# Performance work log

Hardware: AMD Instinct MI355X
Metric: run time of the kernel (lower is better)

Reference implementation:

```python
import jax, jax.numpy as jnp
import numpy as np
import math

BS, C, NH, NL, NP = 2, 128, 1, 2, 8
SHAPES = np.array([[128, 256], [64, 128]], dtype=np.int64)  # [num_level, (H, W)]
NQ = int(SHAPES[0, 0] * SHAPES[0, 1])  # 32768 queries at level-0 resolution
NV = int((SHAPES[:, 0] * SHAPES[:, 1]).sum())  # 40960


def _offset_bias():
    # replicate init_weights grid bias
    thetas = np.arange(NH, dtype=np.float32) * (2.0 * math.pi / NH)
    grid = np.stack([np.cos(thetas), np.sin(thetas)], -1)
    grid = grid / np.abs(grid).max(-1, keepdims=True)
    grid = np.tile(grid.reshape(NH, 1, 1, 2), (1, NL, NP, 1))
    for i in range(NP):
        grid[:, :, i, :] *= i + 1
    return jnp.asarray(grid.reshape(-1), dtype=jnp.float32)


def setup_inputs() -> dict:
    key = jax.random.key(0)
    ks = jax.random.split(key, 8)
    query = jax.random.normal(ks[0], (BS, NQ, C), dtype=jnp.float32)
    value = jax.random.normal(ks[1], (BS, NV, C), dtype=jnp.float32)
    query_location = jax.random.uniform(ks[2], (BS, NQ, NL, 2), dtype=jnp.float32)
    spatial_shapes = jnp.asarray(SHAPES)
    level_start_index = jnp.asarray(np.concatenate([[0], np.cumsum(SHAPES[:, 0] * SHAPES[:, 1])[:-1]]))
    # params (small random offset weights instead of exact-zero init so offsets depend on query)
    W_off = 0.01 * jax.random.normal(ks[3], (C, NH * NL * NP * 2), dtype=jnp.float32)
    b_off = _offset_bias()
    W_attn = 0.01 * jax.random.normal(ks[4], (C, NH * NL * NP), dtype=jnp.float32)
    b_attn = jnp.zeros((NH * NL * NP,), dtype=jnp.float32)
    lim = 1.0 / np.sqrt(C)
    W_out = jax.random.uniform(ks[5], (C * NH, C), minval=-lim, maxval=lim, dtype=jnp.float32)
    b_out = jnp.zeros((C,), dtype=jnp.float32)
    return {"query": query, "value": value, "query_location": query_location,
            "spatial_shapes": spatial_shapes, "level_start_index": level_start_index,
            "W_off": W_off, "b_off": b_off, "W_attn": W_attn, "b_attn": b_attn,
            "W_out": W_out, "b_out": b_out}


def _ms_deform_attn(value, shapes_np, loc, aw):
    # value: [bs, nv, c]; loc: [bs, nq, nh, nl, np, 2] in [0,1]; aw: [bs, nq, nh, nl, np]
    bs, nq = loc.shape[0], loc.shape[1]
    hd = value.shape[-1] // NH
    out = jnp.zeros((bs, NH, nq, hd), dtype=value.dtype)
    start = 0
    for l in range(NL):
        H, W = int(shapes_np[l, 0]), int(shapes_np[l, 1])
        # [bs, nh, H*W, hd]
        v = value[:, start:start + H * W].reshape(bs, H * W, NH, hd).transpose(0, 2, 1, 3)
        # grid_sample align_corners=False convention: x = gx*W - 0.5 with gx in [0,1]
        x = loc[:, :, :, l, :, 0] * W - 0.5  # [bs, nq, nh, np]
        y = loc[:, :, :, l, :, 1] * H - 0.5
        x0 = jnp.floor(x); y0 = jnp.floor(y)
        lx = (x - x0).transpose(0, 2, 1, 3).reshape(bs, NH, nq * NP)[..., None]
        ly = (y - y0).transpose(0, 2, 1, 3).reshape(bs, NH, nq * NP)[..., None]
        x0i = x0.astype(jnp.int32); y0i = y0.astype(jnp.int32)

        def gat(ix, iy):
            valid = ((ix >= 0) & (ix < W) & (iy >= 0) & (iy < H)).astype(value.dtype)
            idx = jnp.clip(iy, 0, H - 1) * W + jnp.clip(ix, 0, W - 1)
            idx_t = idx.transpose(0, 2, 1, 3).reshape(bs, NH, nq * NP)
            g = jnp.take_along_axis(v, idx_t[..., None], axis=2)  # [bs, nh, nq*np, hd]
            m = valid.transpose(0, 2, 1, 3).reshape(bs, NH, nq * NP)
            return g * m[..., None]

        samp = (gat(x0i, y0i) * (1 - lx) * (1 - ly)
                + gat(x0i + 1, y0i) * lx * (1 - ly)
                + gat(x0i, y0i + 1) * (1 - lx) * ly
                + gat(x0i + 1, y0i + 1) * lx * ly)  # [bs, nh, nq*np, hd]
        w = aw[:, :, :, l].transpose(0, 2, 1, 3).reshape(bs, NH, nq * NP)[..., None]
        out = out + (samp * w).reshape(bs, NH, nq, NP, hd).sum(3)
        start += H * W
    return out.transpose(0, 2, 1, 3).reshape(bs, nq, NH * hd)


def reference(query, value, query_location, spatial_shapes, level_start_index,
              W_off, b_off, W_attn, b_attn, W_out, b_out):
    bs, nq, c = query.shape
    shapes_np = np.asarray(spatial_shapes)
    off = (query @ W_off + b_off).reshape(bs, nq, NH, NL, NP, 2)
    aw = jax.nn.softmax((query @ W_attn + b_attn).reshape(bs, nq, NH, NL * NP), axis=-1)
    aw = aw.reshape(bs, nq, NH, NL, NP)
    # offset_normalizer = [W, H] per level
    norm = jnp.stack([jnp.asarray(shapes_np[:, 1], jnp.float32),
                      jnp.asarray(shapes_np[:, 0], jnp.float32)], -1)  # [nl, 2]
    loc = query_location[:, :, None, :, None, :] + off / norm[None, None, None, :, None, :]
    out = _ms_deform_attn(value, shapes_np, loc, aw)
    return out @ W_out + b_out  # dropout is identity at eval
```

## Files before the change

### kernel.cpp

```cpp
#include <hip/hip_runtime.h>
#include <hip/hip_fp16.h>


#define QB 32

struct __align__(8) h2x2 { __half2 a, b; };

typedef _Float16 f16x8 __attribute__((ext_vector_type(8)));
typedef _Float16 f16x4 __attribute__((ext_vector_type(4)));
typedef float    f32x4 __attribute__((ext_vector_type(4)));

__global__ __launch_bounds__(256) void cvt_value_f16_kernel(
    const float4* __restrict__ in, h2x2* __restrict__ out, int n4)
{
    const int i = blockIdx.x * 256 + threadIdx.x;
    if (i < n4) {
        const float4 f = in[i];
        h2x2 h;
        h.a = __floats2half2_rn(f.x, f.y);
        h.b = __floats2half2_rn(f.z, f.w);
        out[i] = h;
    }
}

__global__ __launch_bounds__(256) void wout_transpose_kernel(
    const float* __restrict__ Wout, _Float16* __restrict__ wTg)
{
    __shared__ float t[128 * 129];
    const int tid = threadIdx.x;
    #pragma unroll
    for (int i = 0; i < 16; ++i) {
        const int f  = tid + i * 256;
        const int k  = f >> 5;
        const int c4 = f & 31;
        const float4 v = ((const float4*)Wout)[k * 32 + c4];
        t[k * 129 + c4 * 4 + 0] = v.x;
        t[k * 129 + c4 * 4 + 1] = v.y;
        t[k * 129 + c4 * 4 + 2] = v.z;
        t[k * 129 + c4 * 4 + 3] = v.w;
    }
    __syncthreads();
    #pragma unroll
    for (int i = 0; i < 64; ++i) {
        const int f = tid + i * 256;
        const int n = f >> 7;
        const int k = f & 127;
        wTg[n * 128 + k] = (_Float16)t[k * 129 + n];
    }
}

#define MSDA_PROLOGUE                                                          \
    float* q_tile = (float*)smem_u;                                            \
    int4*  tab    = (int4*)smem_u;                                             \
    const int tid = threadIdx.x;                                               \
    const int r0  = blockIdx.x * QB;                                           \
    {                                                                          \
        const float4* src = (const float4*)query + (size_t)r0 * 32;            \
        float4* dst = (float4*)q_tile;                                         \
        _Pragma("unroll")                                                      \
        for (int i = 0; i < 4; ++i)                                            \
            dst[tid + i * 256] = src[tid + i * 256];                           \
    }                                                                          \
    __syncthreads();                                                           \
    {                                                                          \
        const int jo = tid & 31;                                               \
        const int qb = (tid >> 5) * 4;                                         \
        float s[4] = {0.f, 0.f, 0.f, 0.f};                                     \
        for (int c4 = 0; c4 < 32; ++c4) {                                      \
            const float w0 = Woff[(c4 * 4 + 0) * 32 + jo];                     \
            const float w1 = Woff[(c4 * 4 + 1) * 32 + jo];                     \
            const float w2 = Woff[(c4 * 4 + 2) * 32 + jo];                     \
            const float w3 = Woff[(c4 * 4 + 3) * 32 + jo];                     \
            _Pragma("unroll")                                                  \
            for (int k = 0; k < 4; ++k) {                                      \
                const float4 q4 = *(const float4*)&q_tile[(qb + k) * 128 + c4 * 4]; \
                s[k] += q4.x * w0 + q4.y * w1 + q4.z * w2 + q4.w * w3;         \
            }                                                                  \
        }                                                                      \
        const int l = jo >> 4;                                                 \
        const int d = jo & 1;                                                  \
        const float scale = (d == 0) ? (l == 0 ? 256.f : 128.f)                \
                                     : (l == 0 ? 128.f : 64.f);                \
        const float bo = boff[jo];                                             \
        _Pragma("unroll")                                                      \
        for (int k = 0; k < 4; ++k) {                                          \
            const int row = r0 + qb + k;                                       \
            const float ql = qloc[row * 4 + l * 2 + d];                        \
            coords[(qb + k) * 32 + jo] = ql * scale + (s[k] + bo) - 0.5f;      \
        }                                                                      \
    }                                                                          \
    float wgt_[2];                                                             \
    {                                                                          \
        const int ja = tid & 15;                                               \
        const int qg = tid >> 4;                        \
        float s[2] = {0.f, 0.f};                                               \
        for (int c4 = 0; c4 < 32; ++c4) {                                      \
            const float w0 = Wattn[(c4 * 4 + 0) * 16 + ja];                    \
            const float w1 = Wattn[(c4 * 4 + 1) * 16 + ja];                    \
            const float w2 = Wattn[(c4 * 4 + 2) * 16 + ja];                    \
            const float w3 = Wattn[(c4 * 4 + 3) * 16 + ja];                    \
            _Pragma("unroll")                                                  \
            for (int k = 0; k < 2; ++k) {                                      \
                const float4 q4 = *(const float4*)&q_tile[(qg + 16 * k) * 128 + c4 * 4]; \
                s[k] += q4.x * w0 + q4.y * w1 + q4.z * w2 + q4.w * w3;         \
            }                                                                  \
        }                                                                      \
        const float ba = battn[ja];                                            \
        float lg0 = s[0] + ba, lg1 = s[1] + ba;                                \
        float m0 = lg0, m1 = lg1;                                              \
        _Pragma("unroll")                                                      \
        for (int s_ = 1; s_ < 16; s_ <<= 1) {                                  \
            m0 = fmaxf(m0, __shfl_xor(m0, s_, 64));                            \
            m1 = fmaxf(m1, __shfl_xor(m1, s_, 64));                            \
        }                                                                      \
        const float ex0 = __expf(lg0 - m0), ex1 = __expf(lg1 - m1);            \
        float sm0 = ex0, sm1 = ex1;                                            \
        _Pragma("unroll")                                                      \
        for (int s_ = 1; s_ < 16; s_ <<= 1) {                                  \
            sm0 += __shfl_xor(sm0, s_, 64);                                    \
            sm1 += __shfl_xor(sm1, s_, 64);                                    \
        }                                                                      \
        wgt_[0] = ex0 / sm0;                                                   \
        wgt_[1] = ex1 / sm1;                                                   \
    }                                                                          \
    __syncthreads();    \
    _Pragma("unroll")                                                          \
    for (int k = 0; k < 2; ++k) {                                              \
        const int q = (tid >> 4) + 16 * k;                                     \
        const int p = tid & 15;                                                \
        const int l = p >> 3;                                                  \
        const int H = l ? 64 : 128;                                            \
        const int W = l ? 128 : 256;                                           \
        const int S = l ? 32768 : 0;                                           \
        const float x   = coords[q * 32 + p * 2 + 0];                          \
        const float y   = coords[q * 32 + p * 2 + 1];                          \
        const float wgt = wgt_[k];                                             \
        const float xf = floorf(x), yf = floorf(y);                            \
        const float lx = x - xf, ly = y - yf;                                  \
        const int x0 = (int)xf, y0 = (int)yf;                                  \
        const int x1 = x0 + 1, y1 = y0 + 1;                                    \
        const float hx = 1.f - lx, hy = 1.f - ly;                              \
        float w00 = wgt * hx * hy;                                             \
        float w10 = wgt * lx * hy;                                             \
        float w01 = wgt * hx * ly;                                             \
        float w11 = wgt * lx * ly;                                             \
        if (x0 < 0 || x0 >= W) { w00 = 0.f; w01 = 0.f; }                       \
        if (x1 < 0 || x1 >= W) { w10 = 0.f; w11 = 0.f; }                       \
        if (y0 < 0 || y0 >= H) { w00 = 0.f; w10 = 0.f; }                       \
        if (y1 < 0 || y1 >= H) { w01 = 0.f; w11 = 0.f; }                       \
        const int cx0 = min(max(x0, 0), W - 1);                                \
        const int cx1 = min(max(x1, 0), W - 1);                                \
        const int cy0 = min(max(y0, 0), H - 1);                                \
        const int cy1 = min(max(y1, 0), H - 1);                                \
        int4 e0, e1;                                                           \
        e0.x = __float_as_int(w00); e0.y = __float_as_int(w01);                \
        e0.z = (S + cy0 * W + cx0) * 32; e0.w = (S + cy1 * W + cx0) * 32;      \
        e1.x = __float_as_int(w10); e1.y = __float_as_int(w11);                \
        e1.z = (S + cy0 * W + cx1) * 32; e1.w = (S + cy1 * W + cx1) * 32;      \
        const int e_ = q * 16 + p;                                             \
        tab[e_ * 2]     = e0;                                                  \
        tab[e_ * 2 + 1] = e1;                                                  \
    }                                                                          \
    __syncthreads();

__global__ __launch_bounds__(256, 4) void msda_gather_f16_kernel(
    const float* __restrict__ query,
    const h2x2*  __restrict__ value_h,
    const float* __restrict__ qloc,
    const float* __restrict__ Woff,
    const float* __restrict__ boff,
    const float* __restrict__ Wattn,
    const float* __restrict__ battn,
    float* __restrict__ acc_out)
{
    __shared__ __align__(16) char smem_u[QB * 128 * 4];
    __shared__ float coords[QB * 32];
    MSDA_PROLOGUE

    {
        const int wv   = tid >> 6;
        const int lane = tid & 63;
        const int half = lane >> 5;
        const int cl   = lane & 31;
        const h2x2* vb = value_h + (size_t)(blockIdx.x >> 10) * (40960 * 32);
        float4* og = (float4*)acc_out;

        #pragma unroll 1
        for (int i = 0; i < 8; ++i) {
            const int q = wv * 8 + i;
            float ax = 0.f, ay = 0.f, az = 0.f, aw4 = 0.f;

            #pragma unroll 1
            for (int p0 = 0; p0 < 16; p0 += 8) {
                float wa[8], wb[8];
                int   oa[8], ob[8];
                #pragma unroll
                for (int pi = 0; pi < 8; ++pi) {
                    const int4 t = tab[((q * 16 + p0 + pi) << 1) + half];
                    wa[pi] = __int_as_float(t.x);
                    wb[pi] = __int_as_float(t.y);
                    oa[pi] = t.z + cl;
                    ob[pi] = t.w + cl;
                }
                h2x2 vA[8], vB[8];
                #pragma unroll
                for (int pi = 0; pi < 8; ++pi) {
                    vA[pi] = vb[oa[pi]];
                    vB[pi] = vb[ob[pi]];
                }
                __builtin_amdgcn_sched_barrier(0);
                #pragma unroll
                for (int pi = 0; pi < 8; ++pi) {
                    ax  += wa[pi] * __low2float(vA[pi].a);
                    ay  += wa[pi] * __high2float(vA[pi].a);
                    az  += wa[pi] * __low2float(vA[pi].b);
                    aw4 += wa[pi] * __high2float(vA[pi].b);
                    ax  += wb[pi] * __low2float(vB[pi].a);
                    ay  += wb[pi] * __high2float(vB[pi].a);
                    az  += wb[pi] * __low2float(vB[pi].b);
                    aw4 += wb[pi] * __high2float(vB[pi].b);
                }
            }
            ax  += __shfl_xor(ax, 32, 64);
            ay  += __shfl_xor(ay, 32, 64);
            az  += __shfl_xor(az, 32, 64);
            aw4 += __shfl_xor(aw4, 32, 64);
            if (half == 0)
                og[(size_t)(r0 + q) * 32 + cl] = make_float4(ax, ay, az, aw4);
        }
    }
}

__global__ __launch_bounds__(256, 4) void msda_gather_f32_kernel(
    const float* __restrict__ query,
    const float* __restrict__ value,
    const float* __restrict__ qloc,
    const float* __restrict__ Woff,
    const float* __restrict__ boff,
    const float* __restrict__ Wattn,
    const float* __restrict__ battn,
    float* __restrict__ acc_out)
{
    __shared__ __align__(16) char smem_u[QB * 128 * 4];
    __shared__ float coords[QB * 32];
    MSDA_PROLOGUE

    {
        const int wv   = tid >> 6;
        const int lane = tid & 63;
        const int half = lane >> 5;
        const int cl   = lane & 31;
        const float4* vb = (const float4*)value
                         + (size_t)(blockIdx.x >> 10) * (40960 * 32);
        float4* og = (float4*)acc_out;

        #pragma unroll 1
        for (int i = 0; i < 8; ++i) {
            const int q = wv * 8 + i;
            float ax = 0.f, ay = 0.f, az = 0.f, aw4 = 0.f;

            #pragma unroll 1
            for (int p0 = 0; p0 < 16; p0 += 8) {
                float wa[8], wb[8];
                int   oa[8], ob[8];
                #pragma unroll
                for (int pi = 0; pi < 8; ++pi) {
                    const int4 t = tab[((q * 16 + p0 + pi) << 1) + half];
                    wa[pi] = __int_as_float(t.x);
                    wb[pi] = __int_as_float(t.y);
                    oa[pi] = t.z + cl;
                    ob[pi] = t.w + cl;
                }
                float4 vA[8], vB[8];
                #pragma unroll
                for (int pi = 0; pi < 8; ++pi) {
                    vA[pi] = vb[oa[pi]];
                    vB[pi] = vb[ob[pi]];
                }
                __builtin_amdgcn_sched_barrier(0);
                #pragma unroll
                for (int pi = 0; pi < 8; ++pi) {
                    ax  += wa[pi] * vA[pi].x + wb[pi] * vB[pi].x;
                    ay  += wa[pi] * vA[pi].y + wb[pi] * vB[pi].y;
                    az  += wa[pi] * vA[pi].z + wb[pi] * vB[pi].z;
                    aw4 += wa[pi] * vA[pi].w + wb[pi] * vB[pi].w;
                }
            }
            ax  += __shfl_xor(ax, 32, 64);
            ay  += __shfl_xor(ay, 32, 64);
            az  += __shfl_xor(az, 32, 64);
            aw4 += __shfl_xor(aw4, 32, 64);
            if (half == 0)
                og[(size_t)(r0 + q) * 32 + cl] = make_float4(ax, ay, az, aw4);
        }
    }
}

__global__ __launch_bounds__(256, 2) void msda_out_gemm_mfma_kernel(
    const _Float16* __restrict__ wTg,
    const float* __restrict__ bout,
    float* __restrict__ out)
{
    __shared__ _Float16 aT[128 * 136];
    __shared__ _Float16 wT[128 * 136];
    const int tid = threadIdx.x;
    const int m0  = blockIdx.x * 128;

    #pragma unroll
    for (int i = 0; i < 8; ++i) {
        const int t  = tid + i * 256;
        const int n  = t >> 4;
        const int k8 = t & 15;
        *(f16x8*)&wT[n * 136 + k8 * 8] = *(const f16x8*)&wTg[n * 128 + k8 * 8];
    }
    {
        const float4* src = (const float4*)out;
        #pragma unroll
        for (int i = 0; i < 16; ++i) {
            const int t  = tid + i * 256;
            const int r  = t >> 5;
            const int c4 = t & 31;
            const float4 v = src[(size_t)(m0 + r) * 32 + c4];
            f16x4 h;
            h[0] = (_Float16)v.x; h[1] = (_Float16)v.y;
            h[2] = (_Float16)v.z; h[3] = (_Float16)v.w;
            *(f16x4*)&aT[r * 136 + c4 * 4] = h;
        }
    }
    __syncthreads();

    const int wv   = tid >> 6;
    const int lane = tid & 63;
    const int quad = lane >> 4;
    const int lr   = lane & 15;

    f32x4 acc_[2][8];
    #pragma unroll
    for (int mt = 0; mt < 2; ++mt)
        #pragma unroll
        for (int nt = 0; nt < 8; ++nt)
            acc_[mt][nt] = (f32x4){0.f, 0.f, 0.f, 0.f};

    #pragma unroll
    for (int k0 = 0; k0 < 128; k0 += 32) {
        const f16x8 a0 = *(const f16x8*)&aT[(wv * 32 +  0 + lr) * 136 + k0 + quad * 8];
        const f16x8 a1 = *(const f16x8*)&aT[(wv * 32 + 16 + lr) * 136 + k0 + quad * 8];
        #pragma unroll
        for (int nt = 0; nt < 8; ++nt) {
            const f16x8 b = *(const f16x8*)&wT[(nt * 16 + lr) * 136 + k0 + quad * 8];
            acc_[0][nt] = __builtin_amdgcn_mfma_f32_16x16x32_f16(a0, b, acc_[0][nt], 0, 0, 0);
            acc_[1][nt] = __builtin_amdgcn_mfma_f32_16x16x32_f16(a1, b, acc_[1][nt], 0, 0, 0);
        }
    }

    #pragma unroll
    for (int nt = 0; nt < 8; ++nt) {
        const float bb = bout[nt * 16 + lr];
        #pragma unroll
        for (int mt = 0; mt < 2; ++mt) {
            #pragma unroll
            for (int reg = 0; reg < 4; ++reg) {
                const int row = m0 + wv * 32 + mt * 16 + quad * 4 + reg;
                out[(size_t)row * 128 + nt * 16 + lr] = acc_[mt][nt][reg] + bb;
            }
        }
    }
}

#define GR 128
__global__ __launch_bounds__(256, 2) void msda_out_gemm_f32_kernel(
    const float* __restrict__ Wout,
    const float* __restrict__ bout,
    float* __restrict__ out)
{
    __shared__ __align__(16) float a_tile[GR * 68];
    __shared__ __align__(16) float w_tile[64 * 128];
    const int tid  = threadIdx.x;
    const int r0   = blockIdx.x * GR;
    const int trow = tid >> 4;
    const int tcol = tid & 15;

    float4 o[8][2];
    #pragma unroll
    for (int k = 0; k < 8; ++k) {
        o[k][0] = make_float4(0.f, 0.f, 0.f, 0.f);
        o[k][1] = make_float4(0.f, 0.f, 0.f, 0.f);
    }

    #pragma unroll 1
    for (int h = 0; h < 2; ++h) {
        {
            const float4* src = (const float4*)out;
            #pragma unroll
            for (int i = 0; i < 8; ++i) {
                const int t  = tid + i * 256;
                const int r  = t >> 4;
                const int c4 = t & 15;
                const float4 v = src[(size_t)(r0 + r) * 32 + h * 16 + c4];
                *(float4*)&a_tile[r * 68 + c4 * 4] = v;
            }
            const float4* ws = (const float4*)Wout + (size_t)h * 64 * 32;
            float4* wd = (float4*)w_tile;
            #pragma unroll
            for (int i = 0; i < 8; ++i)
                wd[tid + i * 256] = ws[tid + i * 256];
        }
        __syncthreads();

        #pragma unroll 1
        for (int c4 = 0; c4 < 16; ++c4) {
            float4 a4[8];
            #pragma unroll
            for (int k = 0; k < 8; ++k)
                a4[k] = *(const float4*)&a_tile[(trow + 16 * k) * 68 + c4 * 4];
            #pragma unroll
            for (int j = 0; j < 4; ++j) {
                const int ci = c4 * 4 + j;
                const float4 w0 = *(const float4*)&w_tile[ci * 128 + tcol * 4];
                const float4 w1 = *(const float4*)&w_tile[ci * 128 + 64 + tcol * 4];
                #pragma unroll
                for (int k = 0; k < 8; ++k) {
                    const float a = (j == 0) ? a4[k].x : (j == 1) ? a4[k].y
                                  : (j == 2) ? a4[k].z : a4[k].w;
                    o[k][0].x += a * w0.x; o[k][0].y += a * w0.y;
                    o[k][0].z += a * w0.z; o[k][0].w += a * w0.w;
                    o[k][1].x += a * w1.x; o[k][1].y += a * w1.y;
                    o[k][1].z += a * w1.z; o[k][1].w += a * w1.w;
                }
            }
        }
        __syncthreads();
    }

    const float4 b0 = ((const float4*)bout)[tcol];
    const float4 b1 = ((const float4*)bout)[16 + tcol];
    float4* og = (float4*)out;
    #pragma unroll
    for (int k = 0; k < 8; ++k) {
        const size_t row = (size_t)(r0 + trow + 16 * k);
        float4 v0 = o[k][0], v1 = o[k][1];
        v0.x += b0.x; v0.y += b0.y; v0.z += b0.z; v0.w += b0.w;
        v1.x += b1.x; v1.y += b1.y; v1.z += b1.z; v1.w += b1.w;
        og[row * 32 + tcol]      = v0;
        og[row * 32 + 16 + tcol] = v1;
    }
}

extern "C" void kernel_launch(void* const* d_in, const int* in_sizes, int n_in,
                              void* d_out, int out_size, void* d_ws, size_t ws_size,
                              hipStream_t stream) {
    const float* query = (const float*)d_in[0];
    const float* value = (const float*)d_in[1];
    const float* qloc  = (const float*)d_in[2];
    const float* Woff  = (const float*)d_in[5];
    const float* boff  = (const float*)d_in[6];
    const float* Wattn = (const float*)d_in[7];
    const float* battn = (const float*)d_in[8];
    const float* Wout  = (const float*)d_in[9];
    const float* bout  = (const float*)d_in[10];
    float* out = (float*)d_out;

    const int n_val = 2 * 40960 * 128;
    const size_t f16_bytes = (size_t)n_val * 2;
    const size_t wT_bytes  = 128 * 128 * 2;

    if (ws_size >= f16_bytes + wT_bytes) {
        h2x2* val16 = (h2x2*)d_ws;
        _Float16* wTg = (_Float16*)((char*)d_ws + f16_bytes);
        const int n4 = n_val / 4;
        hipLaunchKernelGGL(cvt_value_f16_kernel, dim3((n4 + 255) / 256), dim3(256),
                           0, stream, (const float4*)value, val16, n4);
        hipLaunchKernelGGL(wout_transpose_kernel, dim3(1), dim3(256), 0, stream,
                           Wout, wTg);
        hipLaunchKernelGGL(msda_gather_f16_kernel, dim3(65536 / QB), dim3(256),
                           0, stream,
                           query, (const h2x2*)val16, qloc, Woff, boff, Wattn, battn, out);
        hipLaunchKernelGGL(msda_out_gemm_mfma_kernel, dim3(65536 / 128), dim3(256),
                           0, stream, (const _Float16*)wTg, bout, out);
    } else if (ws_size >= f16_bytes) {
        h2x2* val16 = (h2x2*)d_ws;
        const int n4 = n_val / 4;
        hipLaunchKernelGGL(cvt_value_f16_kernel, dim3((n4 + 255) / 256), dim3(256),
                           0, stream, (const float4*)value, val16, n4);
        hipLaunchKernelGGL(msda_gather_f16_kernel, dim3(65536 / QB), dim3(256),
                           0, stream,
                           query, (const h2x2*)val16, qloc, Woff, boff, Wattn, battn, out);
        hipLaunchKernelGGL(msda_out_gemm_f32_kernel, dim3(65536 / GR), dim3(256),
                           0, stream, Wout, bout, out);
    } else {
        hipLaunchKernelGGL(msda_gather_f32_kernel, dim3(65536 / QB), dim3(256),
                           0, stream,
                           query, value, qloc, Woff, boff, Wattn, battn, out);
        hipLaunchKernelGGL(msda_out_gemm_f32_kernel, dim3(65536 / GR), dim3(256),
                           0, stream, Wout, bout, out);
    }
}
```

Before: 229.3 us.

## Fuse Wout transpose into value conversion and shrink output GEMM tiles

```diff
diff --git a/kernel.cpp b/kernel.cpp
--- a/kernel.cpp
+++ b/kernel.cpp
@@ -23,29 +23,44 @@
     }
 }
 
-__global__ __launch_bounds__(256) void wout_transpose_kernel(
+__global__ __launch_bounds__(256) void cvt_value_f16_wt_kernel(
+    const float4* __restrict__ in, h2x2* __restrict__ out, int n4,
     const float* __restrict__ Wout, _Float16* __restrict__ wTg)
 {
-    __shared__ float t[128 * 129];
+    __shared__ float t[32 * 129];
     const int tid = threadIdx.x;
-    #pragma unroll
-    for (int i = 0; i < 16; ++i) {
-        const int f  = tid + i * 256;
-        const int k  = f >> 5;
-        const int c4 = f & 31;
-        const float4 v = ((const float4*)Wout)[k * 32 + c4];
-        t[k * 129 + c4 * 4 + 0] = v.x;
-        t[k * 129 + c4 * 4 + 1] = v.y;
-        t[k * 129 + c4 * 4 + 2] = v.z;
-        t[k * 129 + c4 * 4 + 3] = v.w;
-    }
-    __syncthreads();
-    #pragma unroll
-    for (int i = 0; i < 64; ++i) {
-        const int f = tid + i * 256;
-        const int n = f >> 7;
-        const int k = f & 127;
-        wTg[n * 128 + k] = (_Float16)t[k * 129 + n];
+    const int i = blockIdx.x * 256 + tid;
+    if (i < n4) {
+        const float4 f = in[i];
+        h2x2 h;
+        h.a = __floats2half2_rn(f.x, f.y);
+        h.b = __floats2half2_rn(f.z, f.w);
+        out[i] = h;
+        return;
+    }
+    if (blockIdx.x != (unsigned)(n4 / 256)) return;
+    #pragma unroll 1
+    for (int c = 0; c < 4; ++c) {
+        #pragma unroll
+        for (int ii = 0; ii < 4; ++ii) {
+            const int f  = tid + ii * 256;
+            const int r  = f >> 5;
+            const int c4 = f & 31;
+            const float4 v = ((const float4*)Wout)[(c * 32 + r) * 32 + c4];
+            t[r * 129 + c4 * 4 + 0] = v.x;
+            t[r * 129 + c4 * 4 + 1] = v.y;
+            t[r * 129 + c4 * 4 + 2] = v.z;
+            t[r * 129 + c4 * 4 + 3] = v.w;
+        }
+        __syncthreads();
+        #pragma unroll
+        for (int ii = 0; ii < 16; ++ii) {
+            const int f = tid + ii * 256;
+            const int n = f >> 5;
+            const int r = f & 31;
+            wTg[n * 128 + c * 32 + r] = (_Float16)t[r * 129 + n];
+        }
+        __syncthreads();
     }
 }
 
@@ -296,72 +311,64 @@
     }
 }
 
-__global__ __launch_bounds__(256, 2) void msda_out_gemm_mfma_kernel(
+__global__ __launch_bounds__(256, 4) void msda_out_gemm_mfma_kernel(
     const _Float16* __restrict__ wTg,
     const float* __restrict__ bout,
     float* __restrict__ out)
 {
-    __shared__ _Float16 aT[128 * 136];
-    __shared__ _Float16 wT[128 * 136];
-    const int tid = threadIdx.x;
-    const int m0  = blockIdx.x * 128;
-
-    #pragma unroll
-    for (int i = 0; i < 8; ++i) {
-        const int t  = tid + i * 256;
-        const int n  = t >> 4;
-        const int k8 = t & 15;
-        *(f16x8*)&wT[n * 136 + k8 * 8] = *(const f16x8*)&wTg[n * 128 + k8 * 8];
-    }
-    {
-        const float4* src = (const float4*)out;
-        #pragma unroll
-        for (int i = 0; i < 16; ++i) {
-            const int t  = tid + i * 256;
-            const int r  = t >> 5;
-            const int c4 = t & 31;
-            const float4 v = src[(size_t)(m0 + r) * 32 + c4];
-            f16x4 h;
-            h[0] = (_Float16)v.x; h[1] = (_Float16)v.y;
-            h[2] = (_Float16)v.z; h[3] = (_Float16)v.w;
-            *(f16x4*)&aT[r * 136 + c4 * 4] = h;
-        }
-    }
-    __syncthreads();
-
+    const int tid  = threadIdx.x;
+    const int m0   = blockIdx.x * 32;
     const int wv   = tid >> 6;
     const int lane = tid & 63;
     const int quad = lane >> 4;
     const int lr   = lane & 15;
 
-    f32x4 acc_[2][8];
+    f16x8 afrag[2][4];
+    #pragma unroll
+    for (int mt = 0; mt < 2; ++mt) {
+        const float* arow = out + (size_t)(m0 + mt * 16 + lr) * 128;
+        #pragma unroll
+        for (int k = 0; k < 4; ++k) {
+            const float4 v0 = *(const float4*)&arow[k * 32 + quad * 8];
+            const float4 v1 = *(const float4*)&arow[k * 32 + quad * 8 + 4];
+            f16x8 h;
+            h[0] = (_Float16)v0.x; h[1] = (_Float16)v0.y;
+            h[2] = (_Float16)v0.z; h[3] = (_Float16)v0.w;
+            h[4] = (_Float16)v1.x; h[5] = (_Float16)v1.y;
+            h[6] = (_Float16)v1.z; h[7] = (_Float16)v1.w;
+            afrag[mt][k] = h;
+        }
+    }
+    __syncthreads();
+
+    f32x4 acc_[2][2];
     #pragma unroll
     for (int mt = 0; mt < 2; ++mt)
         #pragma unroll
-        for (int nt = 0; nt < 8; ++nt)
-            acc_[mt][nt] = (f32x4){0.f, 0.f, 0.f, 0.f};
+        for (int n2 = 0; n2 < 2; ++n2)
+            acc_[mt][n2] = (f32x4){0.f, 0.f, 0.f, 0.f};
 
     #pragma unroll
-    for (int k0 = 0; k0 < 128; k0 += 32) {
-        const f16x8 a0 = *(const f16x8*)&aT[(wv * 32 +  0 + lr) * 136 + k0 + quad * 8];
-        const f16x8 a1 = *(const f16x8*)&aT[(wv * 32 + 16 + lr) * 136 + k0 + quad * 8];
+    for (int n2 = 0; n2 < 2; ++n2) {
+        const int nt = wv * 2 + n2;
         #pragma unroll
-        for (int nt = 0; nt < 8; ++nt) {
-            const f16x8 b = *(const f16x8*)&wT[(nt * 16 + lr) * 136 + k0 + quad * 8];
-            acc_[0][nt] = __builtin_amdgcn_mfma_f32_16x16x32_f16(a0, b, acc_[0][nt], 0, 0, 0);
-            acc_[1][nt] = __builtin_amdgcn_mfma_f32_16x16x32_f16(a1, b, acc_[1][nt], 0, 0, 0);
+        for (int k = 0; k < 4; ++k) {
+            const f16x8 b = *(const f16x8*)&wTg[(nt * 16 + lr) * 128 + k * 32 + quad * 8];
+            acc_[0][n2] = __builtin_amdgcn_mfma_f32_16x16x32_f16(afrag[0][k], b, acc_[0][n2], 0, 0, 0);
+            acc_[1][n2] = __builtin_amdgcn_mfma_f32_16x16x32_f16(afrag[1][k], b, acc_[1][n2], 0, 0, 0);
         }
     }
 
     #pragma unroll
-    for (int nt = 0; nt < 8; ++nt) {
+    for (int n2 = 0; n2 < 2; ++n2) {
+        const int nt = wv * 2 + n2;
         const float bb = bout[nt * 16 + lr];
         #pragma unroll
         for (int mt = 0; mt < 2; ++mt) {
             #pragma unroll
             for (int reg = 0; reg < 4; ++reg) {
-                const int row = m0 + wv * 32 + mt * 16 + quad * 4 + reg;
-                out[(size_t)row * 128 + nt * 16 + lr] = acc_[mt][nt][reg] + bb;
+                const int row = m0 + mt * 16 + quad * 4 + reg;
+                out[(size_t)row * 128 + nt * 16 + lr] = acc_[mt][n2][reg] + bb;
             }
         }
     }
@@ -468,14 +475,12 @@
         h2x2* val16 = (h2x2*)d_ws;
         _Float16* wTg = (_Float16*)((char*)d_ws + f16_bytes);
         const int n4 = n_val / 4;
-        hipLaunchKernelGGL(cvt_value_f16_kernel, dim3((n4 + 255) / 256), dim3(256),
-                           0, stream, (const float4*)value, val16, n4);
-        hipLaunchKernelGGL(wout_transpose_kernel, dim3(1), dim3(256), 0, stream,
-                           Wout, wTg);
+        hipLaunchKernelGGL(cvt_value_f16_wt_kernel, dim3(n4 / 256 + 1), dim3(256),
+                           0, stream, (const float4*)value, val16, n4, Wout, wTg);
         hipLaunchKernelGGL(msda_gather_f16_kernel, dim3(65536 / QB), dim3(256),
                            0, stream,
                            query, (const h2x2*)val16, qloc, Woff, boff, Wattn, battn, out);
-        hipLaunchKernelGGL(msda_out_gemm_mfma_kernel, dim3(65536 / 128), dim3(256),
+        hipLaunchKernelGGL(msda_out_gemm_mfma_kernel, dim3(65536 / 32), dim3(256),
                            0, stream, (const _Float16*)wTg, bout, out);
     } else if (ws_size >= f16_bytes) {
         h2x2* val16 = (h2x2*)d_ws;
```

New measurement: 250.1 us. 9.1% more time.
